# Optimization experiments

Measured on AMD Instinct MI355X. Metric: run time of the kernel, lower is better.

Reference implementation:

```python
import jax, jax.numpy as jnp
import numpy as np

B, S, D, H = 2, 2048, 1024, 16
DEPTH = D // H


def setup_inputs() -> dict:
    key = jax.random.key(0)
    ks = jax.random.split(key, 8)
    w_scale = 0.02
    # causal mask: 1.0 where attention is NOT allowed (added as mask * -1e9)
    causal = jnp.triu(jnp.ones((S, S), dtype=jnp.float32), k=1)[None, None]  # [1,1,S,S]
    return {
        "q": jax.random.normal(ks[0], (B, S, D), dtype=jnp.float32),
        "k": jax.random.normal(ks[1], (B, S, D), dtype=jnp.float32),
        "v": jax.random.normal(ks[2], (B, S, D), dtype=jnp.float32),
        "mask": causal,
        "Wq": jax.random.normal(ks[3], (D, D), dtype=jnp.float32) * w_scale,
        "bq": jnp.zeros((D,), dtype=jnp.float32),
        "Wk": jax.random.normal(ks[4], (D, D), dtype=jnp.float32) * w_scale,
        "bk": jnp.zeros((D,), dtype=jnp.float32),
        "Wv": jax.random.normal(ks[5], (D, D), dtype=jnp.float32) * w_scale,
        "bv": jnp.zeros((D,), dtype=jnp.float32),
        "Wo": jax.random.normal(ks[6], (D, D), dtype=jnp.float32) * w_scale,
        "bo": jnp.zeros((D,), dtype=jnp.float32),
    }


def _split_heads(x):
    # [B,S,D] -> [B,H,S,depth]
    return x.reshape(B, S, H, DEPTH).transpose(0, 2, 1, 3)


def reference(q, k, v, mask, Wq, bq, Wk, bk, Wv, bv, Wo, bo):
    qh = _split_heads(q @ Wq + bq)
    kh = _split_heads(k @ Wk + bk)
    vh = _split_heads(v @ Wv + bv)
    scale = 1.0 / jnp.sqrt(jnp.asarray(DEPTH, dtype=qh.dtype))
    logits = jnp.einsum('bhqd,bhkd->bhqk', qh, kh) * scale  # [B,H,S,S]
    logits = logits + mask * (-1e9)
    attn = jax.nn.softmax(logits, axis=-1)
    out = jnp.einsum('bhqk,bhkd->bhqd', attn, vh)  # [B,H,S,depth]
    out = out.transpose(0, 2, 1, 3).reshape(B, S, D)
    return out @ Wo + bo
```

## Files before the change

### kernel.cpp

```cpp
#include <hip/hip_runtime.h>


typedef unsigned short u16;
typedef unsigned int u32;

using bf16x8 = __attribute__((ext_vector_type(8))) short;
using f32x4  = __attribute__((ext_vector_type(4))) float;

#define SEQ 2048
#define DMODEL 1024
#define NHEAD 16
#define DEPTH 64
#define BATCH 2
#define M_ROWS (BATCH * SEQ)

__device__ __forceinline__ u16 f2bf(float f) {
    union { float f; u32 u; } v; v.f = f;
    u32 u = v.u;
    return (u16)((u + 0x7FFFu + ((u >> 16) & 1u)) >> 16);
}
__device__ __forceinline__ u16 f2bf_trunc(float f) {
    union { float f; u32 u; } v; v.f = f;
    return (u16)(v.u >> 16);
}

__device__ __forceinline__ f32x4 mfma16(bf16x8 a, bf16x8 b, f32x4 c) {
    return __builtin_amdgcn_mfma_f32_16x16x32_bf16(a, b, c, 0, 0, 0);
}

__device__ __forceinline__ void glds16(const u16* src, u16* dst) {
    __builtin_amdgcn_global_load_lds((const __attribute__((address_space(1))) void*)src,
                                     (__attribute__((address_space(3))) void*)dst,
                                     16, 0, 0);
}

__device__ __forceinline__ bf16x8 fragld(const u16* base, int lr, int gc) {
    return *(const bf16x8*)(base + lr * 64 + (((gc ^ lr) & 7) << 3));
}

__global__ void cvt3_kernel(const float* __restrict__ q, const float* __restrict__ k,
                            const float* __restrict__ v,
                            u16* __restrict__ qo, u16* __restrict__ ko, u16* __restrict__ vo) {
    const float* in; u16* out;
    if (blockIdx.z == 0)      { in = q; out = qo; }
    else if (blockIdx.z == 1) { in = k; out = ko; }
    else                      { in = v; out = vo; }
    int idx = blockIdx.x * blockDim.x + threadIdx.x;
    float4 val = ((const float4*)in)[idx];
    ushort4 o;
    o.x = f2bf(val.x); o.y = f2bf(val.y); o.z = f2bf(val.z); o.w = f2bf(val.w);
    ((ushort4*)out)[idx] = o;
}

__global__ void wtrans_kernel(const float* __restrict__ Wq, const float* __restrict__ Wk,
                              const float* __restrict__ Wv, const float* __restrict__ Wo,
                              u16* __restrict__ Wqt, u16* __restrict__ Wkt,
                              u16* __restrict__ Wvt, u16* __restrict__ Wot) {
    __shared__ float tile[32][33];
    const float* W; u16* Wt;
    switch (blockIdx.z) {
        case 0: W = Wq; Wt = Wqt; break;
        case 1: W = Wk; Wt = Wkt; break;
        case 2: W = Wv; Wt = Wvt; break;
        default: W = Wo; Wt = Wot; break;
    }
    int k0 = blockIdx.x * 32, n0 = blockIdx.y * 32;
    int tx = threadIdx.x, ty = threadIdx.y;
#pragma unroll
    for (int i = 0; i < 4; ++i)
        tile[ty + 8 * i][tx] = W[(size_t)(k0 + ty + 8 * i) * DMODEL + n0 + tx];
    __syncthreads();
#pragma unroll
    for (int i = 0; i < 4; ++i)
        Wt[(size_t)(n0 + ty + 8 * i) * DMODEL + k0 + tx] = f2bf(tile[tx][ty + 8 * i]);
}

template<int TM>
__device__ __forceinline__ void gemm_core(const u16* __restrict__ A, const u16* __restrict__ Bt,
                                          const float* __restrict__ bias,
                                          u16* __restrict__ outb, float* __restrict__ outf,
                                          int mode, float oscale, int bm0, int bn0) {
    constexpr int K = DMODEL;
    constexpr int NT = K / 64;
    constexpr int MI = TM / 32;
    __shared__ u16 As[2][TM * 64];
    __shared__ u16 Bs[2][128 * 64];
    int t = threadIdx.x;
    int w = t >> 6, lane = t & 63, l15 = lane & 15, quad = lane >> 4;
    int wm = (w >> 1) * (TM / 2), wn = (w & 1) * 64;
    int r8 = lane >> 3, g8 = lane & 7;
    int gswz = ((g8 ^ r8) << 3);
    f32x4 acc[MI][4] = {};

#define QSTAGE(p, kt) do { \
    _Pragma("unroll") for (int c = 0; c < MI; ++c) { \
        int ch = w * MI + c; \
        glds16(A + (size_t)(bm0 + ch * 8 + r8) * K + (kt) * 64 + gswz, &As[p][ch * 512]); } \
    _Pragma("unroll") for (int c = 0; c < 4; ++c) { \
        int ch = w * 4 + c; \
        glds16(Bt + (size_t)(bn0 + ch * 8 + r8) * K + (kt) * 64 + gswz, &Bs[p][ch * 512]); } \
    } while (0)

    QSTAGE(0, 0);
    __syncthreads();

    for (int kt = 0; kt < NT; ++kt) {
        int cur = kt & 1;
        if (kt + 1 < NT) QSTAGE(cur ^ 1, kt + 1);
#pragma unroll
        for (int kk = 0; kk < 2; ++kk) {
            bf16x8 af[MI], bfr[4];
#pragma unroll
            for (int i = 0; i < MI; ++i) af[i]  = fragld(&As[cur][0], wm + i * 16 + l15, kk * 4 + quad);
#pragma unroll
            for (int j = 0; j < 4;  ++j) bfr[j] = fragld(&Bs[cur][0], wn + j * 16 + l15, kk * 4 + quad);
#pragma unroll
            for (int i = 0; i < MI; ++i)
#pragma unroll
                for (int j = 0; j < 4; ++j)
                    acc[i][j] = mfma16(af[i], bfr[j], acc[i][j]);
        }
        __syncthreads();
    }
#undef QSTAGE

#pragma unroll
    for (int i = 0; i < MI; ++i) {
        int row_g0 = bm0 + wm + i * 16 + quad * 4;
#pragma unroll
        for (int j = 0; j < 4; ++j) {
            int col_g = bn0 + wn + j * 16 + l15;
            float bsv = bias[col_g];
#pragma unroll
            for (int r = 0; r < 4; ++r) {
                float v = (acc[i][j][r] + bsv) * oscale;
                int rg = row_g0 + r;
                if (mode == 2) {
                    outf[(size_t)rg * DMODEL + col_g] = v;
                } else {
                    int b = rg >> 11, s = rg & (SEQ - 1);
                    int h = col_g >> 6, d = col_g & 63;
                    size_t idx;
                    if (mode == 0) idx = ((size_t)(b * NHEAD + h) * SEQ + s) * DEPTH + d;
                    else           idx = ((size_t)(b * NHEAD + h) * DEPTH + d) * SEQ + s;
                    outb[idx] = f2bf(v);
                }
            }
        }
    }
}

#define SCALE_Q 0.1803368801111204f

__global__ __launch_bounds__(256) void gemm_qkv(
        const u16* __restrict__ qb, const u16* __restrict__ kb, const u16* __restrict__ vb,
        const u16* __restrict__ Wqt, const u16* __restrict__ Wkt, const u16* __restrict__ Wvt,
        const float* __restrict__ bq, const float* __restrict__ bk, const float* __restrict__ bv,
        u16* __restrict__ Qp, u16* __restrict__ Kp, u16* __restrict__ Vpt) {
    int id = blockIdx.x;
    int c = id & 7, m = id >> 3;
    int slab = c * 12 + (m >> 3);
    int x = m & 7;
    int z = slab >> 5, y = slab & 31;
    int bm0 = y * 128, bn0 = x * 128;
    if (z == 0)      gemm_core<128>(qb, Wqt, bq, Qp,  nullptr, 0, SCALE_Q, bm0, bn0);
    else if (z == 1) gemm_core<128>(kb, Wkt, bk, Kp,  nullptr, 0, 1.0f,    bm0, bn0);
    else             gemm_core<128>(vb, Wvt, bv, Vpt, nullptr, 1, 1.0f,    bm0, bn0);
}

__global__ __launch_bounds__(256) void gemm_out(
        const u16* __restrict__ attnb, const u16* __restrict__ Wot,
        const float* __restrict__ bo, float* __restrict__ out) {
    int id = blockIdx.x;
    int c = id & 7, m = id >> 3;
    int slab = c * 8 + (m >> 3);
    int x = m & 7;
    gemm_core<64>(attnb, Wot, bo, nullptr, out, 2, 1.0f, slab * 64, x * 128);
}

#define LP 72
__global__ __launch_bounds__(256) void attn_kernel(
        const u16* __restrict__ Qp, const u16* __restrict__ Kp,
        const u16* __restrict__ Vpt, u16* __restrict__ attn_out, u32* __restrict__ ctrs) {
    __shared__ u16 Klds[2][64 * 64];
    __shared__ u16 Vtlds[2][64 * 64];
    __shared__ u16 Plds[4 * 16 * LP];
    __shared__ u32 item_s;
    int t = threadIdx.x, w = t >> 6, lane = t & 63, l15 = lane & 15, quad = lane >> 4;
    int r8 = lane >> 3, g8 = lane & 7;
    int gswz = ((g8 ^ r8) << 3);
    u16* Pw = Plds + w * 16 * LP;
    int xcd = blockIdx.x & 7;
    u32* my_ctr = ctrs + xcd * 32;

    bf16x8 ones;
#pragma unroll
    for (int i = 0; i < 8; ++i) ones[i] = (short)0x3F80;

    for (;;) {
        if (t == 0) item_s = atomicAdd(my_ctr, 1);
        __syncthreads();
        u32 item = item_s;
        if (item >= 128) break;
        int qt = 31 - (int)(item >> 2);
        int bh = xcd * 4 + (int)(item & 3);
        int q0 = qt * 64;
        int nkt = qt + 1;
        int b = bh >> 4, h = bh & 15;
        const u16* Qbase = Qp  + (size_t)bh * SEQ * DEPTH;
        const u16* Kbase = Kp  + (size_t)bh * SEQ * DEPTH;
        const u16* Vbase = Vpt + (size_t)bh * DEPTH * SEQ;

        int qrow = q0 + w * 16 + l15;
        bf16x8 qf[2];
        qf[0] = *(const bf16x8*)(Qbase + (size_t)qrow * DEPTH + quad * 8);
        qf[1] = *(const bf16x8*)(Qbase + (size_t)qrow * DEPTH + 32 + quad * 8);

        f32x4 of[4] = {};
        f32x4 lacc = {};

#pragma unroll
        for (int c2 = 0; c2 < 2; ++c2) {
            int ch = w * 2 + c2;
            glds16(Kbase + (size_t)(ch * 8 + r8) * DEPTH + gswz, Klds[0] + ch * 512);
            glds16(Vbase + (size_t)(ch * 8 + r8) * SEQ + gswz,   Vtlds[0] + ch * 512);
        }

        for (int kt = 0; kt < nkt; ++kt) {
            int cur = kt & 1;
            __syncthreads();
            if (kt + 1 < nkt) {
                int nx = cur ^ 1, kn = kt + 1;
#pragma unroll
                for (int c2 = 0; c2 < 2; ++c2) {
                    int ch = w * 2 + c2;
                    glds16(Kbase + (size_t)(kn * 64 + ch * 8 + r8) * DEPTH + gswz,
                           Klds[nx] + ch * 512);
                    glds16(Vbase + (size_t)(ch * 8 + r8) * SEQ + kn * 64 + gswz,
                           Vtlds[nx] + ch * 512);
                }
            }
            f32x4 sc[4] = {};
#pragma unroll
            for (int nt = 0; nt < 4; ++nt)
#pragma unroll
                for (int kk = 0; kk < 2; ++kk)
                    sc[nt] = mfma16(qf[kk], fragld(Klds[cur], nt * 16 + l15, kk * 4 + quad), sc[nt]);

            bool diag = (kt == nkt - 1);
#pragma unroll
            for (int nt = 0; nt < 4; ++nt) {
#pragma unroll
                for (int r = 0; r < 4; ++r) {
                    float e = exp2f(sc[nt][r]);
                    if (diag) {
                        int col = nt * 16 + l15, row_ = w * 16 + quad * 4 + r;
                        e = (col > row_) ? 0.f : e;
                    }
                    Pw[(quad * 4 + r) * LP + nt * 16 + l15] = f2bf_trunc(e);
                }
            }
            bf16x8 pf[2];
            pf[0] = *(const bf16x8*)(Pw + l15 * LP + quad * 8);
            pf[1] = *(const bf16x8*)(Pw + l15 * LP + 32 + quad * 8);
#pragma unroll
            for (int kk = 0; kk < 2; ++kk) {
                lacc = mfma16(pf[kk], ones, lacc);
#pragma unroll
                for (int nt = 0; nt < 4; ++nt)
                    of[nt] = mfma16(pf[kk], fragld(Vtlds[cur], nt * 16 + l15, kk * 4 + quad), of[nt]);
            }
        }
#pragma unroll
        for (int r = 0; r < 4; ++r) {
            float inv = 1.0f / lacc[r];
            int s_ = q0 + w * 16 + quad * 4 + r;
#pragma unroll
            for (int nt = 0; nt < 4; ++nt) {
                int dcol = h * DEPTH + nt * 16 + l15;
                attn_out[((size_t)(b * SEQ + s_)) * DMODEL + dcol] = f2bf(of[nt][r] * inv);
            }
        }
    }
}

extern "C" void kernel_launch(void* const* d_in, const int* in_sizes, int n_in,
                              void* d_out, int out_size, void* d_ws, size_t ws_size,
                              hipStream_t stream) {
    const float* q  = (const float*)d_in[0];
    const float* k  = (const float*)d_in[1];
    const float* v  = (const float*)d_in[2];
    const float* Wq = (const float*)d_in[4];
    const float* bq = (const float*)d_in[5];
    const float* Wk = (const float*)d_in[6];
    const float* bk = (const float*)d_in[7];
    const float* Wv = (const float*)d_in[8];
    const float* bv = (const float*)d_in[9];
    const float* Wo = (const float*)d_in[10];
    const float* bo = (const float*)d_in[11];
    float* out = (float*)d_out;

    char* ws = (char*)d_ws;
    const size_t SZ_ACT = (size_t)M_ROWS * DMODEL * 2;
    const size_t SZ_W   = (size_t)DMODEL * DMODEL * 2;
    u16* qb   = (u16*)(ws);
    u16* kb   = (u16*)(ws + SZ_ACT);
    u16* vb   = (u16*)(ws + 2 * SZ_ACT);
    u16* Wqt  = (u16*)(ws + 3 * SZ_ACT);
    u16* Wkt  = (u16*)(ws + 3 * SZ_ACT + SZ_W);
    u16* Wvt  = (u16*)(ws + 3 * SZ_ACT + 2 * SZ_W);
    u16* Wot  = (u16*)(ws + 3 * SZ_ACT + 3 * SZ_W);
    u16* Qp   = (u16*)(ws + 3 * SZ_ACT + 4 * SZ_W);
    u16* Kp   = (u16*)(ws + 4 * SZ_ACT + 4 * SZ_W);
    u16* Vpt  = (u16*)(ws + 5 * SZ_ACT + 4 * SZ_W);
    u16* attnb= (u16*)(ws + 6 * SZ_ACT + 4 * SZ_W);
    u32* ctrs = (u32*)(ws + 7 * SZ_ACT + 4 * SZ_W);

    hipMemsetAsync(ctrs, 0, 1024, stream);
    cvt3_kernel<<<dim3(4096, 1, 3), 256, 0, stream>>>(q, k, v, qb, kb, vb);
    wtrans_kernel<<<dim3(32, 32, 4), dim3(32, 8), 0, stream>>>(Wq, Wk, Wv, Wo, Wqt, Wkt, Wvt, Wot);
    gemm_qkv<<<dim3(768), 256, 0, stream>>>(
        qb, kb, vb, Wqt, Wkt, Wvt, bq, bk, bv, Qp, Kp, Vpt);
    attn_kernel<<<dim3(768), 256, 0, stream>>>(Qp, Kp, Vpt, attnb, ctrs);
    gemm_out<<<dim3(512), 256, 0, stream>>>(attnb, Wot, bo, out);
}
```

Baseline: 246.7 us.

## Halve GEMM K-tile, add occupancy hints, transpose QK^T for vectorized P stores

The projection GEMM core now stages 32-wide K tiles instead of 64, which halves shared memory per block, uses a 4-way swizzle, and issues a single MFMA k-step per iteration. Both GEMM kernels gain __launch_bounds__(256,4) to target higher occupancy. In attention, the score MFMA operands are swapped so each lane holds a key column for a single query row, which lets the probability tile be written to LDS as 4-wide vector stores instead of scalar stores. The trade-off is twice as many K-loop iterations and barriers in the GEMMs, plus register pressure limits imposed by the occupancy hint.

Result: faster. 227.3 us (-7.9%).

```diff
diff --git a/kernel.cpp b/kernel.cpp
--- a/kernel.cpp
+++ b/kernel.cpp
@@ -5,6 +5,7 @@
 typedef unsigned int u32;
 
 using bf16x8 = __attribute__((ext_vector_type(8))) short;
+using bf16x4 = __attribute__((ext_vector_type(4))) short;
 using f32x4  = __attribute__((ext_vector_type(4))) float;
 
 #define SEQ 2048
@@ -36,6 +37,9 @@
 
 __device__ __forceinline__ bf16x8 fragld(const u16* base, int lr, int gc) {
     return *(const bf16x8*)(base + lr * 64 + (((gc ^ lr) & 7) << 3));
+}
+__device__ __forceinline__ bf16x8 fragld32(const u16* base, int lr, int gc) {
+    return *(const bf16x8*)(base + lr * 32 + (((gc ^ lr) & 3) << 3));
 }
 
 __global__ void cvt3_kernel(const float* __restrict__ q, const float* __restrict__ k,
@@ -81,24 +85,25 @@
                                           u16* __restrict__ outb, float* __restrict__ outf,
                                           int mode, float oscale, int bm0, int bn0) {
     constexpr int K = DMODEL;
-    constexpr int NT = K / 64;
+    constexpr int NT = K / 32;
     constexpr int MI = TM / 32;
-    __shared__ u16 As[2][TM * 64];
-    __shared__ u16 Bs[2][128 * 64];
+    constexpr int ACH = TM / 64;
+    __shared__ u16 As[2][TM * 32];
+    __shared__ u16 Bs[2][128 * 32];
     int t = threadIdx.x;
     int w = t >> 6, lane = t & 63, l15 = lane & 15, quad = lane >> 4;
     int wm = (w >> 1) * (TM / 2), wn = (w & 1) * 64;
-    int r8 = lane >> 3, g8 = lane & 7;
-    int gswz = ((g8 ^ r8) << 3);
+    int r16 = lane >> 2, g4 = lane & 3;
+    int gswz = ((g4 ^ (r16 & 3)) << 3);
     f32x4 acc[MI][4] = {};
 
 #define QSTAGE(p, kt) do { \
-    _Pragma("unroll") for (int c = 0; c < MI; ++c) { \
-        int ch = w * MI + c; \
-        glds16(A + (size_t)(bm0 + ch * 8 + r8) * K + (kt) * 64 + gswz, &As[p][ch * 512]); } \
-    _Pragma("unroll") for (int c = 0; c < 4; ++c) { \
-        int ch = w * 4 + c; \
-        glds16(Bt + (size_t)(bn0 + ch * 8 + r8) * K + (kt) * 64 + gswz, &Bs[p][ch * 512]); } \
+    _Pragma("unroll") for (int c = 0; c < ACH; ++c) { \
+        int ch = w * ACH + c; \
+        glds16(A + (size_t)(bm0 + ch * 16 + r16) * K + (kt) * 32 + gswz, &As[p][ch * 512]); } \
+    _Pragma("unroll") for (int c = 0; c < 2; ++c) { \
+        int ch = w * 2 + c; \
+        glds16(Bt + (size_t)(bn0 + ch * 16 + r16) * K + (kt) * 32 + gswz, &Bs[p][ch * 512]); } \
     } while (0)
 
     QSTAGE(0, 0);
@@ -107,19 +112,16 @@
     for (int kt = 0; kt < NT; ++kt) {
         int cur = kt & 1;
         if (kt + 1 < NT) QSTAGE(cur ^ 1, kt + 1);
-#pragma unroll
-        for (int kk = 0; kk < 2; ++kk) {
-            bf16x8 af[MI], bfr[4];
-#pragma unroll
-            for (int i = 0; i < MI; ++i) af[i]  = fragld(&As[cur][0], wm + i * 16 + l15, kk * 4 + quad);
-#pragma unroll
-            for (int j = 0; j < 4;  ++j) bfr[j] = fragld(&Bs[cur][0], wn + j * 16 + l15, kk * 4 + quad);
-#pragma unroll
-            for (int i = 0; i < MI; ++i)
-#pragma unroll
-                for (int j = 0; j < 4; ++j)
-                    acc[i][j] = mfma16(af[i], bfr[j], acc[i][j]);
-        }
+        bf16x8 af[MI], bfr[4];
+#pragma unroll
+        for (int i = 0; i < MI; ++i) af[i]  = fragld32(&As[cur][0], wm + i * 16 + l15, quad);
+#pragma unroll
+        for (int j = 0; j < 4;  ++j) bfr[j] = fragld32(&Bs[cur][0], wn + j * 16 + l15, quad);
+#pragma unroll
+        for (int i = 0; i < MI; ++i)
+#pragma unroll
+            for (int j = 0; j < 4; ++j)
+                acc[i][j] = mfma16(af[i], bfr[j], acc[i][j]);
         __syncthreads();
     }
 #undef QSTAGE
@@ -152,7 +154,7 @@
 
 #define SCALE_Q 0.1803368801111204f
 
-__global__ __launch_bounds__(256) void gemm_qkv(
+__global__ __launch_bounds__(256, 4) void gemm_qkv(
         const u16* __restrict__ qb, const u16* __restrict__ kb, const u16* __restrict__ vb,
         const u16* __restrict__ Wqt, const u16* __restrict__ Wkt, const u16* __restrict__ Wvt,
         const float* __restrict__ bq, const float* __restrict__ bk, const float* __restrict__ bv,
@@ -168,7 +170,7 @@
     else             gemm_core<128>(vb, Wvt, bv, Vpt, nullptr, 1, 1.0f,    bm0, bn0);
 }
 
-__global__ __launch_bounds__(256) void gemm_out(
+__global__ __launch_bounds__(256, 4) void gemm_out(
         const u16* __restrict__ attnb, const u16* __restrict__ Wot,
         const float* __restrict__ bo, float* __restrict__ out) {
     int id = blockIdx.x;
@@ -240,26 +242,30 @@
                            Vtlds[nx] + ch * 512);
                 }
             }
-            f32x4 sc[4] = {};
+            f32x4 st[4] = {};
 #pragma unroll
             for (int nt = 0; nt < 4; ++nt)
 #pragma unroll
                 for (int kk = 0; kk < 2; ++kk)
-                    sc[nt] = mfma16(qf[kk], fragld(Klds[cur], nt * 16 + l15, kk * 4 + quad), sc[nt]);
+                    st[nt] = mfma16(fragld(Klds[cur], nt * 16 + l15, kk * 4 + quad), qf[kk], st[nt]);
 
             bool diag = (kt == nkt - 1);
+            int qlv = w * 16 + l15;
 #pragma unroll
             for (int nt = 0; nt < 4; ++nt) {
+                bf16x4 pv;
 #pragma unroll
                 for (int r = 0; r < 4; ++r) {
-                    float e = exp2f(sc[nt][r]);
+                    float e = exp2f(st[nt][r]);
                     if (diag) {
-                        int col = nt * 16 + l15, row_ = w * 16 + quad * 4 + r;
-                        e = (col > row_) ? 0.f : e;
+                        int keyl = nt * 16 + quad * 4 + r;
+                        e = (keyl > qlv) ? 0.f : e;
                     }
-                    Pw[(quad * 4 + r) * LP + nt * 16 + l15] = f2bf_trunc(e);
+                    pv[r] = (short)f2bf_trunc(e);
                 }
-            }
+                *(bf16x4*)(Pw + l15 * LP + nt * 16 + quad * 4) = pv;
+            }
+            asm volatile("" ::: "memory");
             bf16x8 pf[2];
             pf[0] = *(const bf16x8*)(Pw + l15 * LP + quad * 8);
             pf[1] = *(const bf16x8*)(Pw + l15 * LP + 32 + quad * 8);
```
